# Optimization experiments

Measured on AMD Instinct MI355X. Metric: run time of the kernel, lower is better.

Reference implementation:

```python
import jax, jax.numpy as jnp
import numpy as np

B = 64          # batch of graphs
N_GOALS = 16
N_SHELVES = 112
N = N_GOALS + N_SHELVES   # 128 nodes per graph
L = 5           # num_layers
D = 32          # node_embedding_dim
DE = 32         # edge_embedding_dim
DT = 32         # timestep_embedding_dim
D_MSG_IN = 2 * D + DT + 1  # 97


def setup_inputs() -> dict:
    key = jax.random.key(0)
    ks = iter(jax.random.split(key, 40))
    def nrm(shape, s=0.05):
        return jax.random.normal(next(ks), shape, jnp.float32) * s
    inp = {}
    inp["pos"] = jax.random.uniform(next(ks), (B, N_SHELVES, 2), jnp.float32, -1.0, 1.0)
    inp["timesteps"] = jax.random.randint(next(ks), (B,), 0, 1000)
    inp["goal_pos"] = jax.random.uniform(next(ks), (N_GOALS, 2), jnp.float32, -1.0, 1.0)
    inp["W_hin"] = nrm((2, D));            inp["b_hin"] = nrm((D,))
    inp["W_msg1"] = nrm((L, D_MSG_IN, DE)); inp["b_msg1"] = nrm((L, DE))
    inp["W_msg2"] = nrm((L, DE, DE));       inp["b_msg2"] = nrm((L, DE))
    inp["W_att"] = nrm((L, DE, 1));         inp["b_att"] = nrm((L, 1))
    inp["W_pos1"] = nrm((L, DE, DE));       inp["b_pos1"] = nrm((L, DE))
    inp["W_pos2"] = nrm((L, DE, 1));        inp["b_pos2"] = nrm((L, 1))
    inp["W_node1"] = nrm((L - 1, DE + D, D)); inp["b_node1"] = nrm((L - 1, D))
    inp["W_node2"] = nrm((L - 1, D, D));      inp["b_node2"] = nrm((L - 1, D))
    inp["W_t"] = nrm((L - 1, DT, DT));        inp["b_t"] = nrm((L - 1, DT))
    return inp


def _forward(pos, timesteps, goal_pos, W_hin, b_hin, W_msg1, b_msg1, W_msg2, b_msg2,
             W_att, b_att, W_pos1, b_pos1, W_pos2, b_pos2,
             W_node1, b_node1, W_node2, b_node2, W_t, b_t):
    silu = jax.nn.silu
    b = pos.shape[0]
    n_g = goal_pos.shape[0]
    n_sh = pos.shape[1]
    n = n_g + n_sh
    num_layers = W_msg1.shape[0]

    # fully-connected edge template per graph (PyG: edge_index[0]=src=row, edge_index[1]=dst=col)
    src_l = jnp.repeat(jnp.arange(n), n)
    dst_l = jnp.tile(jnp.arange(n), n)
    offs = (jnp.arange(b) * n)[:, None]
    src = (offs + src_l[None, :]).reshape(-1)   # [b*n*n]
    dst = (offs + dst_l[None, :]).reshape(-1)
    e_batch = jnp.repeat(jnp.arange(b), n * n)  # batch[edge_index[0]]

    # node one-hot features: goals [1,0], shelves [0,1]
    h0 = jnp.concatenate([
        jnp.tile(jnp.array([1.0, 0.0], jnp.float32), (n_g, 1)),
        jnp.tile(jnp.array([0.0, 1.0], jnp.float32), (n_sh, 1)),
    ], axis=0)                                   # [n, 2]
    x = jnp.tile(h0, (b, 1))                     # [b*n, 2]

    # node positions: goal positions (shared template) then shelf positions
    p = jnp.concatenate([jnp.broadcast_to(goal_pos, (b, n_g, 2)), pos], axis=1).reshape(-1, 2)

    # sinusoidal timestep embedding
    dt = b_t.shape[-1]
    half = dt // 2
    freqs = jnp.exp(-jnp.log(10000.0) * jnp.arange(half, dtype=jnp.float32) / half)
    ang = timesteps.astype(jnp.float32)[:, None] * freqs[None, :]
    temb = jnp.concatenate([jnp.cos(ang), jnp.sin(ang)], axis=-1)  # [b, dt]

    h = x @ W_hin + b_hin  # [b*n, D]

    for i in range(num_layers):
        te = temb[e_batch]                       # [E, dt]
        pd = p[dst] - p[src]                     # pos_i - pos_j
        radial = jnp.sum(pd * pd, axis=-1, keepdims=True)
        pd = pd / (jax.lax.stop_gradient(jnp.sqrt(radial)) + 1e-6)
        m = jnp.concatenate([h[dst], h[src], radial, te], axis=-1)  # [E, 97]
        m = silu(m @ W_msg1[i] + b_msg1[i])
        m = silu(m @ W_msg2[i] + b_msg2[i])
        m = m * jax.nn.sigmoid(m @ W_att[i] + b_att[i])             # attention gate
        pw = silu(m @ W_pos1[i] + b_pos1[i]) @ W_pos2[i] + b_pos2[i]  # [E, 1]
        aggr_h = jax.ops.segment_sum(m, dst, num_segments=b * n)    # scatter-add
        # scatter-mean: every node receives exactly n incoming edges (fully connected incl. self-loop)
        aggr_p = jax.ops.segment_sum(pd * pw, dst, num_segments=b * n) / n
        if i < num_layers - 1:
            u = silu(jnp.concatenate([h, aggr_h], axis=-1) @ W_node1[i] + b_node1[i])
            u = u @ W_node2[i] + b_node2[i]
            h = jnp.where(u > 0, u, 0.01 * u) + h   # LeakyReLU + residual
            temb = silu(temb @ W_t[i] + b_t[i])
        p = aggr_p + p

    return p.reshape(b, n, 2)[:, n_g:, :].reshape(pos.shape)


def reference(pos, timesteps, goal_pos, W_hin, b_hin, W_msg1, b_msg1, W_msg2, b_msg2,
              W_att, b_att, W_pos1, b_pos1, W_pos2, b_pos2,
              W_node1, b_node1, W_node2, b_node2, W_t, b_t):
    return _forward(pos, timesteps, goal_pos, W_hin, b_hin, W_msg1, b_msg1, W_msg2, b_msg2,
                    W_att, b_att, W_pos1, b_pos1, W_pos2, b_pos2,
                    W_node1, b_node1, W_node2, b_node2, W_t, b_t)
```

## Files before the change

kernel.cpp:

```cpp
#include <hip/hip_runtime.h>
#include <hip/hip_bf16.h>

constexpr int B = 64;
constexpr int NG = 16;
constexpr int NSH = 112;
constexpr int N = 128;
constexpr int NN = B * N;
constexpr int L = 5;

constexpr int OFF_H     = 0;
constexpr int OFF_P     = OFF_H + NN * 32;
constexpr int OFF_TEMB0 = OFF_P + NN * 2;
constexpr int OFF_TEMB1 = OFF_TEMB0 + B * 32;
constexpr int OFF_HA    = OFF_TEMB1 + B * 32;
constexpr int OFF_HB    = OFF_HA + NN * 32;
constexpr int OFF_AGH   = OFF_HB + NN * 32;
constexpr int OFF_AGP   = OFF_AGH + NN * 32;

typedef __attribute__((ext_vector_type(8))) short bf16x8;
typedef __attribute__((ext_vector_type(4))) float f32x4;

__device__ __forceinline__ float fsigmoid(float x) {
    return __builtin_amdgcn_rcpf(1.0f + __expf(-x));
}
__device__ __forceinline__ float fsilu(float x) { return x * fsigmoid(x); }
__device__ __forceinline__ short f2bfs(float f) {
    union { __hip_bfloat16 b; short s; } u; u.b = __float2bfloat16(f); return u.s;
}
__device__ __forceinline__ float bf2f(unsigned short u) {
    union { unsigned int i; float f; } v; v.i = ((unsigned int)u) << 16; return v.f;
}
__device__ __forceinline__ unsigned int pk_trunc(float lo, float hi) {
    union { float f; unsigned int u; } a, b;
    a.f = hi; b.f = lo;
    return __builtin_amdgcn_perm(a.u, b.u, 0x07060302u);
}

__global__ __launch_bounds__(256) void setup_kernel(
    const float* __restrict__ pos, const int* __restrict__ timesteps,
    const float* __restrict__ goal_pos,
    const float* __restrict__ W_hin, const float* __restrict__ b_hin,
    float* __restrict__ ws)
{
    int idx = blockIdx.x * 256 + threadIdx.x;

    if (idx < NN * 32) {
        int c = idx & 31; int node = idx >> 5; int local = node & 127;
        int row = (local < NG) ? 0 : 1;
        ws[OFF_H + idx] = W_hin[row * 32 + c] + b_hin[c];
        return;
    }
    idx -= NN * 32;
    if (idx < NN * 2) {
        int d = idx & 1; int node = idx >> 1; int g = node >> 7; int local = node & 127;
        float v = (local < NG) ? goal_pos[local * 2 + d]
                               : pos[(g * NSH + (local - NG)) * 2 + d];
        ws[OFF_P + idx] = v;
        return;
    }
    idx -= NN * 2;
    if (idx < B * 32) {
        int j = idx & 31; int g = idx >> 5;
        float t = (float)timesteps[g];
        int jj = (j < 16) ? j : (j - 16);
        float freq = expf(-logf(10000.0f) * (float)jj / 16.0f);
        float ang = t * freq;
        ws[OFF_TEMB0 + idx] = (j < 16) ? cosf(ang) : sinf(ang);
    }
}

__global__ __launch_bounds__(256) void pre_kernel(
    float* __restrict__ R,
    const float* __restrict__ W_msg1, const float* __restrict__ b_msg1,
    const float* __restrict__ tembIn, int layer)
{
    int tid = blockIdx.x * 256 + threadIdx.x;
    int c = tid & 31; int node = tid >> 5; int g = node >> 7;
    const float* __restrict__ W1 = W_msg1 + layer * 97 * 32;
    float accA = b_msg1[layer * 32 + c];
    float accB = 0.f;
#pragma unroll
    for (int k = 0; k < 32; ++k) {
        float hk = R[OFF_H + node * 32 + k];
        accA += hk * W1[k * 32 + c];
        accB += hk * W1[(32 + k) * 32 + c];
    }
#pragma unroll
    for (int k = 0; k < 32; ++k)
        accA += tembIn[g * 32 + k] * W1[(65 + k) * 32 + c];
    R[OFF_HA + tid] = accA;
    ((unsigned short*)(R + OFF_HB))[tid] = (unsigned short)f2bfs(accB);
}

__global__ __attribute__((amdgpu_flat_work_group_size(256, 256)))
__attribute__((amdgpu_waves_per_eu(2, 4))) void edge_kernel(
    float* __restrict__ R,
    const float* __restrict__ W_msg1,
    const float* __restrict__ W_msg2, const float* __restrict__ b_msg2,
    const float* __restrict__ W_att, const float* __restrict__ b_att,
    const float* __restrict__ W_pos1, const float* __restrict__ b_pos1,
    const float* __restrict__ W_pos2, const float* __restrict__ b_pos2,
    float* __restrict__ aggh, float* __restrict__ aggp, int layer)
{
    __shared__ unsigned short sHBh[128 * 40];
    __shared__ float sPx[128], sPy[128];
    __shared__ unsigned int mbuf[4 * 64 * 20];
    __shared__ float2 spn[4][64];

    const int t = threadIdx.x;
    const int bx = blockIdx.x;
    const int g = bx >> 5;
    const int gbase = g * 128;

    const unsigned short* HBH = (const unsigned short*)(R + OFF_HB);
#pragma unroll
    for (int ch = 0; ch < 2; ++ch) {
        int chunk = t + ch * 256;
        int row = chunk >> 2, g4 = chunk & 3;
        uint4 v = *(const uint4*)(HBH + (gbase + row) * 32 + (g4 << 3));
        *(uint4*)(sHBh + row * 40 + (g4 << 3)) = v;
    }
    if (t < 128) {
        sPx[t] = R[OFF_P + (gbase + t) * 2];
        sPy[t] = R[OFF_P + (gbase + t) * 2 + 1];
    }
    __syncthreads();

    const int lane = t & 63, w = t >> 6;
    const int c = lane & 15;
    const int rg = lane >> 4;
    const int kk = rg << 3;
    const int dloc = ((bx & 31) << 2) | w;
    const int dstNode = gbase + dloc;

    const float* __restrict__ Wm2L = W_msg2 + layer * 1024;
    const float* __restrict__ Wp1L = W_pos1 + layer * 1024;
    bf16x8 WB1c0, WB1c1, WBpc0, WBpc1, WBac;
#pragma unroll
    for (int j = 0; j < 8; ++j) {
        WB1c0[j] = f2bfs(Wm2L[(kk + j) * 32 + c]);
        WB1c1[j] = f2bfs(Wm2L[(kk + j) * 32 + c + 16]);
        int pk = ((kk + j) & 1) * 16 + ((kk + j) >> 1);
        WBpc0[j] = f2bfs(Wp1L[pk * 32 + c]);
        WBpc1[j] = f2bfs(Wp1L[pk * 32 + c + 16]);
        WBac[j]  = f2bfs(W_att[layer * 32 + pk]);
    }

    float vha[8], vwr[8];
    {
        const float* haR = R + OFF_HA + dstNode * 32 + kk;
        const float* wrR = W_msg1 + layer * 97 * 32 + 64 * 32 + kk;
#pragma unroll
        for (int j = 0; j < 8; ++j) { vha[j] = haR[j]; vwr[j] = wrR[j]; }
    }
    const float batt   = b_att[layer];
    const float vbm20  = b_msg2[layer * 32 + c], vbm21 = b_msg2[layer * 32 + c + 16];
    const float vbp10  = b_pos1[layer * 32 + c], vbp11 = b_pos1[layer * 32 + c + 16];
    const float vwp20  = W_pos2[layer * 32 + c], vwp21 = W_pos2[layer * 32 + c + 16];
    const float bp2    = b_pos2[layer];
    const float pxd = R[OFF_P + dstNode * 2], pyd = R[OFF_P + dstNode * 2 + 1];

    unsigned int* mb = mbuf + w * 64 * 20;

    float aghc0 = 0.f, aghc1 = 0.f, apx = 0.f, apy = 0.f, spnx = 0.f, spny = 0.f;

#pragma unroll 1
    for (int half = 0; half < 2; ++half) {
        const int src = (half << 6) + lane;
        const float dx = pxd - sPx[src];
        const float dy = pyd - sPy[src];
        const float radial = dx * dx + dy * dy;
        const float inv = __builtin_amdgcn_rcpf(__builtin_amdgcn_sqrtf(radial) + 1e-6f);
        const float pnx = dx * inv, pny = dy * inv;
        spnx += pnx; spny += pny;
        spn[w][lane] = (float2){pnx, pny};

        f32x4 acc0[4], acc1[4];
#pragma unroll
        for (int tt = 0; tt < 4; ++tt) {
            acc0[tt] = (f32x4){vbm20, vbm20, vbm20, vbm20};
            acc1[tt] = (f32x4){vbm21, vbm21, vbm21, vbm21};
        }
#pragma unroll
        for (int tt = 0; tt < 4; ++tt) {
            const float rad_t = __shfl(radial, c + (tt << 4));
            uint4 hraw = *(const uint4*)(sHBh + ((half << 6) + c + (tt << 4)) * 40 + kk);
            const unsigned short* hs = (const unsigned short*)&hraw;
            float x[8];
#pragma unroll
            for (int j = 0; j < 8; ++j)
                x[j] = fsilu(vha[j] + bf2f(hs[j]) + rad_t * vwr[j]);
            union { unsigned int u[4]; bf16x8 v; } af;
#pragma unroll
            for (int d = 0; d < 4; ++d) af.u[d] = pk_trunc(x[2 * d], x[2 * d + 1]);
            acc0[tt] = __builtin_amdgcn_mfma_f32_16x16x32_bf16(af.v, WB1c0, acc0[tt], 0, 0, 0);
            acc1[tt] = __builtin_amdgcn_mfma_f32_16x16x32_bf16(af.v, WB1c1, acc1[tt], 0, 0, 0);
        }

#pragma unroll
        for (int tt = 0; tt < 4; ++tt)
#pragma unroll
            for (int j = 0; j < 4; ++j) {
                float s0 = fsilu(acc0[tt][j]);
                float s1 = fsilu(acc1[tt][j]);
                acc0[tt][j] = s0; acc1[tt][j] = s1;
                mb[(tt * 16 + rg * 4 + j) * 20 + c] = pk_trunc(s0, s1);
            }

#pragma unroll
        for (int tt = 0; tt < 4; ++tt) {
            union { uint4 u; bf16x8 v; } qa;
            qa.u = *(const uint4*)(mb + (c + (tt << 4)) * 20 + (rg << 2));
            f32x4 za = (f32x4){batt, batt, batt, batt};
            f32x4 z0 = (f32x4){0.f, 0.f, 0.f, 0.f};
            f32x4 z1 = (f32x4){0.f, 0.f, 0.f, 0.f};
            za = __builtin_amdgcn_mfma_f32_16x16x32_bf16(qa.v, WBac,  za, 0, 0, 0);
            z0 = __builtin_amdgcn_mfma_f32_16x16x32_bf16(qa.v, WBpc0, z0, 0, 0, 0);
            z1 = __builtin_amdgcn_mfma_f32_16x16x32_bf16(qa.v, WBpc1, z1, 0, 0, 0);
#pragma unroll
            for (int j = 0; j < 4; ++j) {
                const float att = fsigmoid(za[j]);
                aghc0 += att * acc0[tt][j];
                aghc1 += att * acc1[tt][j];
                const float q0 = fsilu(att * z0[j] + vbp10);
                const float q1 = fsilu(att * z1[j] + vbp11);
                const float pwp = q0 * vwp20 + q1 * vwp21;
                const float2 pn = spn[w][(tt << 4) + (rg << 2) + j];
                apx += pwp * pn.x;
                apy += pwp * pn.y;
            }
        }
    }

    aghc0 += __shfl_xor(aghc0, 16); aghc0 += __shfl_xor(aghc0, 32);
    aghc1 += __shfl_xor(aghc1, 16); aghc1 += __shfl_xor(aghc1, 32);
#pragma unroll
    for (int off = 1; off < 64; off <<= 1) {
        apx  += __shfl_xor(apx, off);
        apy  += __shfl_xor(apy, off);
        spnx += __shfl_xor(spnx, off);
        spny += __shfl_xor(spny, off);
    }
    if (lane < 16)       aggh[dstNode * 32 + lane] = aghc0;
    else if (lane < 32)  aggh[dstNode * 32 + lane] = aghc1;
    if (lane == 0) {
        aggp[dstNode * 2]     = (apx + bp2 * spnx) * (1.0f / 128.0f);
        aggp[dstNode * 2 + 1] = (apy + bp2 * spny) * (1.0f / 128.0f);
    }
}

__global__ __launch_bounds__(256) void node_kernel(
    float* __restrict__ ws,
    const float* __restrict__ W_node1, const float* __restrict__ b_node1,
    const float* __restrict__ W_node2, const float* __restrict__ b_node2,
    const float* __restrict__ W_t, const float* __restrict__ b_t,
    int layer)
{
    __shared__ float sIn[8][64];
    __shared__ float sU1[8][32];

    const int tid = blockIdx.x * 256 + threadIdx.x;
    const int c = tid & 31;
    const int node = tid >> 5;
    const int ln = (threadIdx.x >> 5) & 7;

    const float* __restrict__ Wn1 = W_node1 + layer * 2048;
    const float* __restrict__ Wn2 = W_node2 + layer * 1024;

    sIn[ln][c]      = ws[OFF_H + node * 32 + c];
    sIn[ln][32 + c] = ws[OFF_AGH + node * 32 + c];
    __syncthreads();

    float acc = b_node1[layer * 32 + c];
#pragma unroll
    for (int k = 0; k < 32; ++k)
        acc += sIn[ln][k] * Wn1[k * 32 + c] + sIn[ln][32 + k] * Wn1[(32 + k) * 32 + c];
    sU1[ln][c] = fsilu(acc);
    __syncthreads();

    float u = b_node2[layer * 32 + c];
#pragma unroll
    for (int k = 0; k < 32; ++k) u += sU1[ln][k] * Wn2[k * 32 + c];
    const float hn = (u > 0.f ? u : 0.01f * u) + sIn[ln][c];
    ws[OFF_H + node * 32 + c] = hn;

    if (c < 2)
        ws[OFF_P + node * 2 + c] += ws[OFF_AGP + node * 2 + c];

    if (tid < B * 32) {
        const int g = tid >> 5, c2 = tid & 31;
        const float* Wt = W_t + layer * 1024;
        const float* tin = ws + ((layer & 1) ? OFF_TEMB1 : OFF_TEMB0) + g * 32;
        float acc2 = b_t[layer * 32 + c2];
#pragma unroll
        for (int k = 0; k < 32; ++k) acc2 += tin[k] * Wt[k * 32 + c2];
        ws[((layer & 1) ? OFF_TEMB0 : OFF_TEMB1) + tid] = fsilu(acc2);
    }
}

__global__ __launch_bounds__(256) void out_kernel(const float* __restrict__ R,
                                                  float* __restrict__ out)
{
    const int o = blockIdx.x * 256 + threadIdx.x;
    if (o >= B * NSH * 2) return;
    const int d = o & 1;
    const int s = (o >> 1) % NSH;
    const int b = (o >> 1) / NSH;
    const int node = b * 128 + NG + s;
    out[o] = R[OFF_P + node * 2 + d] + R[OFF_AGP + node * 2 + d];
}

extern "C" void kernel_launch(void* const* d_in, const int* in_sizes, int n_in,
                              void* d_out, int out_size, void* d_ws, size_t ws_size,
                              hipStream_t stream)
{
    const float* pos      = (const float*)d_in[0];
    const int*   tsteps   = (const int*)d_in[1];
    const float* goal_pos = (const float*)d_in[2];
    const float* W_hin    = (const float*)d_in[3];
    const float* b_hin    = (const float*)d_in[4];
    const float* W_msg1   = (const float*)d_in[5];
    const float* b_msg1   = (const float*)d_in[6];
    const float* W_msg2   = (const float*)d_in[7];
    const float* b_msg2   = (const float*)d_in[8];
    const float* W_att    = (const float*)d_in[9];
    const float* b_att    = (const float*)d_in[10];
    const float* W_pos1   = (const float*)d_in[11];
    const float* b_pos1   = (const float*)d_in[12];
    const float* W_pos2   = (const float*)d_in[13];
    const float* b_pos2   = (const float*)d_in[14];
    const float* W_node1  = (const float*)d_in[15];
    const float* b_node1  = (const float*)d_in[16];
    const float* W_node2  = (const float*)d_in[17];
    const float* b_node2  = (const float*)d_in[18];
    const float* W_t      = (const float*)d_in[19];
    const float* b_t      = (const float*)d_in[20];

    float* ws = (float*)d_ws;

    constexpr int setup_threads = NN * 32 + NN * 2 + B * 32;
    setup_kernel<<<(setup_threads + 255) / 256, 256, 0, stream>>>(
        pos, tsteps, goal_pos, W_hin, b_hin, ws);

    for (int l = 0; l < L; ++l) {
        const float* tembIn = ws + ((l & 1) ? OFF_TEMB1 : OFF_TEMB0);
        pre_kernel<<<NN * 32 / 256, 256, 0, stream>>>(ws, W_msg1, b_msg1, tembIn, l);
        edge_kernel<<<2048, 256, 0, stream>>>(ws, W_msg1, W_msg2, b_msg2, W_att, b_att,
                                              W_pos1, b_pos1, W_pos2, b_pos2,
                                              ws + OFF_AGH, ws + OFF_AGP, l);
        if (l < L - 1)
            node_kernel<<<NN * 32 / 256, 256, 0, stream>>>(ws, W_node1, b_node1, W_node2,
                                                           b_node2, W_t, b_t, l);
    }
    out_kernel<<<(B * NSH * 2 + 255) / 256, 256, 0, stream>>>(ws, (float*)d_out);
}
```

Measured before the change: 324.9 us.

## Fuse next-layer pre-projection and temb update into node kernel; shrink edge register tile

The node kernel now also computes the next layer's timestep embedding (once per block, kept in shared memory) and the next layer's message pre-projection (HA/HB), so the separate pre_kernel launch per layer is removed and only the initial one remains. The edge kernel processes each 16-row MFMA tile end to end instead of holding four tiles of accumulators, which shrinks the LDS message buffer and register use. It also targets higher occupancy via waves_per_eu(5). The trade-off is redundant temb computation in every node block and more serial work inside the node kernel.

```diff
diff --git a/kernel.cpp b/kernel.cpp
--- a/kernel.cpp
+++ b/kernel.cpp
@@ -93,7 +93,7 @@
 }
 
 __global__ __attribute__((amdgpu_flat_work_group_size(256, 256)))
-__attribute__((amdgpu_waves_per_eu(2, 4))) void edge_kernel(
+__attribute__((amdgpu_waves_per_eu(5))) void edge_kernel(
     float* __restrict__ R,
     const float* __restrict__ W_msg1,
     const float* __restrict__ W_msg2, const float* __restrict__ b_msg2,
@@ -104,7 +104,7 @@
 {
     __shared__ unsigned short sHBh[128 * 40];
     __shared__ float sPx[128], sPy[128];
-    __shared__ unsigned int mbuf[4 * 64 * 20];
+    __shared__ unsigned int mbuf[4 * 16 * 20];
     __shared__ float2 spn[4][64];
 
     const int t = threadIdx.x;
@@ -160,7 +160,7 @@
     const float bp2    = b_pos2[layer];
     const float pxd = R[OFF_P + dstNode * 2], pyd = R[OFF_P + dstNode * 2 + 1];
 
-    unsigned int* mb = mbuf + w * 64 * 20;
+    unsigned int* mb = mbuf + w * 16 * 20;
 
     float aghc0 = 0.f, aghc1 = 0.f, apx = 0.f, apy = 0.f, spnx = 0.f, spny = 0.f;
 
@@ -175,12 +175,6 @@
         spnx += pnx; spny += pny;
         spn[w][lane] = (float2){pnx, pny};
 
-        f32x4 acc0[4], acc1[4];
-#pragma unroll
-        for (int tt = 0; tt < 4; ++tt) {
-            acc0[tt] = (f32x4){vbm20, vbm20, vbm20, vbm20};
-            acc1[tt] = (f32x4){vbm21, vbm21, vbm21, vbm21};
-        }
 #pragma unroll
         for (int tt = 0; tt < 4; ++tt) {
             const float rad_t = __shfl(radial, c + (tt << 4));
@@ -193,24 +187,21 @@
             union { unsigned int u[4]; bf16x8 v; } af;
 #pragma unroll
             for (int d = 0; d < 4; ++d) af.u[d] = pk_trunc(x[2 * d], x[2 * d + 1]);
-            acc0[tt] = __builtin_amdgcn_mfma_f32_16x16x32_bf16(af.v, WB1c0, acc0[tt], 0, 0, 0);
-            acc1[tt] = __builtin_amdgcn_mfma_f32_16x16x32_bf16(af.v, WB1c1, acc1[tt], 0, 0, 0);
-        }
-
-#pragma unroll
-        for (int tt = 0; tt < 4; ++tt)
+            f32x4 a0 = (f32x4){vbm20, vbm20, vbm20, vbm20};
+            f32x4 a1 = (f32x4){vbm21, vbm21, vbm21, vbm21};
+            a0 = __builtin_amdgcn_mfma_f32_16x16x32_bf16(af.v, WB1c0, a0, 0, 0, 0);
+            a1 = __builtin_amdgcn_mfma_f32_16x16x32_bf16(af.v, WB1c1, a1, 0, 0, 0);
+
+            float s0[4], s1[4];
 #pragma unroll
             for (int j = 0; j < 4; ++j) {
-                float s0 = fsilu(acc0[tt][j]);
-                float s1 = fsilu(acc1[tt][j]);
-                acc0[tt][j] = s0; acc1[tt][j] = s1;
-                mb[(tt * 16 + rg * 4 + j) * 20 + c] = pk_trunc(s0, s1);
+                s0[j] = fsilu(a0[j]);
+                s1[j] = fsilu(a1[j]);
+                mb[((rg << 2) + j) * 20 + c] = pk_trunc(s0[j], s1[j]);
             }
 
-#pragma unroll
-        for (int tt = 0; tt < 4; ++tt) {
             union { uint4 u; bf16x8 v; } qa;
-            qa.u = *(const uint4*)(mb + (c + (tt << 4)) * 20 + (rg << 2));
+            qa.u = *(const uint4*)(mb + c * 20 + (rg << 2));
             f32x4 za = (f32x4){batt, batt, batt, batt};
             f32x4 z0 = (f32x4){0.f, 0.f, 0.f, 0.f};
             f32x4 z1 = (f32x4){0.f, 0.f, 0.f, 0.f};
@@ -220,8 +211,8 @@
 #pragma unroll
             for (int j = 0; j < 4; ++j) {
                 const float att = fsigmoid(za[j]);
-                aghc0 += att * acc0[tt][j];
-                aghc1 += att * acc1[tt][j];
+                aghc0 += att * s0[j];
+                aghc1 += att * s1[j];
                 const float q0 = fsilu(att * z0[j] + vbp10);
                 const float q1 = fsilu(att * z1[j] + vbp11);
                 const float pwp = q0 * vwp20 + q1 * vwp21;
@@ -254,21 +245,27 @@
     const float* __restrict__ W_node1, const float* __restrict__ b_node1,
     const float* __restrict__ W_node2, const float* __restrict__ b_node2,
     const float* __restrict__ W_t, const float* __restrict__ b_t,
+    const float* __restrict__ W_msg1, const float* __restrict__ b_msg1,
     int layer)
 {
     __shared__ float sIn[8][64];
     __shared__ float sU1[8][32];
+    __shared__ float sHn[8][32];
+    __shared__ float sTold[32], sTnew[32];
 
     const int tid = blockIdx.x * 256 + threadIdx.x;
     const int c = tid & 31;
     const int node = tid >> 5;
     const int ln = (threadIdx.x >> 5) & 7;
+    const int g = node >> 7;
 
     const float* __restrict__ Wn1 = W_node1 + layer * 2048;
     const float* __restrict__ Wn2 = W_node2 + layer * 1024;
 
     sIn[ln][c]      = ws[OFF_H + node * 32 + c];
     sIn[ln][32 + c] = ws[OFF_AGH + node * 32 + c];
+    if (threadIdx.x < 32)
+        sTold[threadIdx.x] = ws[((layer & 1) ? OFF_TEMB1 : OFF_TEMB0) + g * 32 + threadIdx.x];
     __syncthreads();
 
     float acc = b_node1[layer * 32 + c];
@@ -276,6 +273,13 @@
     for (int k = 0; k < 32; ++k)
         acc += sIn[ln][k] * Wn1[k * 32 + c] + sIn[ln][32 + k] * Wn1[(32 + k) * 32 + c];
     sU1[ln][c] = fsilu(acc);
+    if (threadIdx.x < 32) {
+        const float* Wt = W_t + layer * 1024;
+        float a2 = b_t[layer * 32 + threadIdx.x];
+#pragma unroll
+        for (int k = 0; k < 32; ++k) a2 += sTold[k] * Wt[k * 32 + threadIdx.x];
+        sTnew[threadIdx.x] = fsilu(a2);
+    }
     __syncthreads();
 
     float u = b_node2[layer * 32 + c];
@@ -283,19 +287,28 @@
     for (int k = 0; k < 32; ++k) u += sU1[ln][k] * Wn2[k * 32 + c];
     const float hn = (u > 0.f ? u : 0.01f * u) + sIn[ln][c];
     ws[OFF_H + node * 32 + c] = hn;
+    sHn[ln][c] = hn;
 
     if (c < 2)
         ws[OFF_P + node * 2 + c] += ws[OFF_AGP + node * 2 + c];
-
-    if (tid < B * 32) {
-        const int g = tid >> 5, c2 = tid & 31;
-        const float* Wt = W_t + layer * 1024;
-        const float* tin = ws + ((layer & 1) ? OFF_TEMB1 : OFF_TEMB0) + g * 32;
-        float acc2 = b_t[layer * 32 + c2];
-#pragma unroll
-        for (int k = 0; k < 32; ++k) acc2 += tin[k] * Wt[k * 32 + c2];
-        ws[((layer & 1) ? OFF_TEMB0 : OFF_TEMB1) + tid] = fsilu(acc2);
-    }
+    if ((blockIdx.x & 15) == 0 && threadIdx.x < 32)
+        ws[((layer & 1) ? OFF_TEMB0 : OFF_TEMB1) + g * 32 + threadIdx.x] = sTnew[threadIdx.x];
+    __syncthreads();
+
+    const float* __restrict__ W1 = W_msg1 + (layer + 1) * 97 * 32;
+    float accA = b_msg1[(layer + 1) * 32 + c];
+    float accB = 0.f;
+#pragma unroll
+    for (int k = 0; k < 32; ++k) {
+        const float hk = sHn[ln][k];
+        accA += hk * W1[k * 32 + c];
+        accB += hk * W1[(32 + k) * 32 + c];
+    }
+#pragma unroll
+    for (int k = 0; k < 32; ++k)
+        accA += sTnew[k] * W1[(65 + k) * 32 + c];
+    ws[OFF_HA + node * 32 + c] = accA;
+    ((unsigned short*)(ws + OFF_HB))[node * 32 + c] = (unsigned short)f2bfs(accB);
 }
 
 __global__ __launch_bounds__(256) void out_kernel(const float* __restrict__ R,
@@ -341,16 +354,15 @@
     constexpr int setup_threads = NN * 32 + NN * 2 + B * 32;
     setup_kernel<<<(setup_threads + 255) / 256, 256, 0, stream>>>(
         pos, tsteps, goal_pos, W_hin, b_hin, ws);
+    pre_kernel<<<NN * 32 / 256, 256, 0, stream>>>(ws, W_msg1, b_msg1, ws + OFF_TEMB0, 0);
 
     for (int l = 0; l < L; ++l) {
-        const float* tembIn = ws + ((l & 1) ? OFF_TEMB1 : OFF_TEMB0);
-        pre_kernel<<<NN * 32 / 256, 256, 0, stream>>>(ws, W_msg1, b_msg1, tembIn, l);
         edge_kernel<<<2048, 256, 0, stream>>>(ws, W_msg1, W_msg2, b_msg2, W_att, b_att,
                                               W_pos1, b_pos1, W_pos2, b_pos2,
                                               ws + OFF_AGH, ws + OFF_AGP, l);
         if (l < L - 1)
             node_kernel<<<NN * 32 / 256, 256, 0, stream>>>(ws, W_node1, b_node1, W_node2,
-                                                           b_node2, W_t, b_t, l);
+                                                           b_node2, W_t, b_t, W_msg1, b_msg1, l);
     }
     out_kernel<<<(B * NSH * 2 + 255) / 256, 256, 0, stream>>>(ws, (float*)d_out);
 }
```

New measurement: 562.0 us. +73.0%, slower.
